# Performance work log

Measured on AMD Instinct MI355X. Metric: run time of the kernel, lower is better.

## Reference

```python
import jax, jax.numpy as jnp
import numpy as np

EPS = 1e-08
ATOM_CA = 1


def setup_inputs() -> dict:
    key = jax.random.key(0)
    k1, k2 = jax.random.split(key)
    B, N_RES, N_ATOMS = 256, 1024, 37
    pred_coords = jax.random.normal(k1, (B, N_RES, N_ATOMS, 3), dtype=jnp.float32)
    true_coords = jax.random.normal(k2, (B, N_RES, N_ATOMS, 3), dtype=jnp.float32)
    atom_mask = jnp.ones((B, N_RES, N_ATOMS), dtype=jnp.float32)
    return {"pred_coords": pred_coords, "true_coords": true_coords, "atom_mask": atom_mask}


def _kabsch_align(pred, true, mask):
    # pred/true: [B, N, 3], mask: [B, N]
    mask_sum = jnp.sum(mask, axis=1, keepdims=True) + EPS          # [B, 1]
    m = mask[..., None]                                             # [B, N, 1]
    pred_center = jnp.sum(pred * m, axis=1) / mask_sum              # [B, 3]
    true_center = jnp.sum(true * m, axis=1) / mask_sum              # [B, 3]
    pred_c = (pred - pred_center[:, None, :]) * m                   # [B, N, 3]
    true_c = (true - true_center[:, None, :]) * m                   # [B, N, 3]
    H = jnp.einsum('bni,bnj->bij', pred_c, true_c)                  # [B, 3, 3]
    U, s, Vh = jnp.linalg.svd(H)                                    # H = U diag(s) Vh
    V = jnp.swapaxes(Vh, -1, -2)
    Ut = jnp.swapaxes(U, -1, -2)
    det = jnp.linalg.det(jnp.matmul(V, Ut))                         # [B]
    sign = jnp.stack([jnp.ones_like(det), jnp.ones_like(det), det], axis=-1)  # [B, 3]
    S = jnp.eye(3, dtype=pred.dtype) * sign[:, None, :]             # diag(1,1,det)
    R = jnp.matmul(jnp.matmul(V, S), Ut)                            # [B, 3, 3]
    # aligned = (pred - pred_center) @ R^T + true_center
    aligned = jnp.einsum('bnj,bij->bni', pred - pred_center[:, None, :], R)
    return aligned + true_center[:, None, :]


def reference(pred_coords, true_coords, atom_mask):
    pred_ca = pred_coords[:, :, ATOM_CA, :]   # [B, N_res, 3]
    true_ca = true_coords[:, :, ATOM_CA, :]
    ca_mask = atom_mask[:, :, ATOM_CA]        # [B, N_res]
    pred_ca = _kabsch_align(pred_ca, true_ca, ca_mask)
    diff_sq = jnp.sum((pred_ca - true_ca) ** 2, axis=-1)            # [B, N_res]
    rmsd = jnp.sqrt(jnp.sum(diff_sq * ca_mask, axis=1) / (jnp.sum(ca_mask, axis=1) + EPS))
    return jnp.mean(rmsd)
```

## Files before the change

kernel.cpp:

```cpp
#include <hip/hip_runtime.h>
#include <math.h>

#define N_RES 1024
#define N_ATOMS 37
#define ATOM_CA 1
#define NBATCH 256
#define NSUM 34

__global__ __launch_bounds__(256) void rmsd_batch_kernel(
    const float* __restrict__ pred, const float* __restrict__ truec,
    const float* __restrict__ mask, float* __restrict__ ws)
{
    const int b = blockIdx.x;
    const int tid = threadIdx.x;

    float acc[NSUM];
#pragma unroll
    for (int i = 0; i < NSUM; ++i) acc[i] = 0.f;

    const size_t resStride = (size_t)N_ATOMS * 3;
    const float* pb = pred  + (size_t)b * N_RES * resStride + ATOM_CA * 3;
    const float* tb = truec + (size_t)b * N_RES * resStride + ATOM_CA * 3;
    const float* mb = mask  + (size_t)b * N_RES * N_ATOMS + ATOM_CA;

    for (int n = tid; n < N_RES; n += 256) {
        const float m  = mb[(size_t)n * N_ATOMS];
        const float* pp = pb + (size_t)n * resStride;
        const float* tt = tb + (size_t)n * resStride;
        const float p0 = pp[0], p1 = pp[1], p2 = pp[2];
        const float t0 = tt[0], t1 = tt[1], t2 = tt[2];
        const float m2 = m * m;
        acc[0] += m;
        acc[1] += m * p0;  acc[2] += m * p1;  acc[3] += m * p2;
        acc[4] += m * t0;  acc[5] += m * t1;  acc[6] += m * t2;
        acc[7] += m * (p0*p0 + p1*p1 + p2*p2);
        acc[8] += m * (t0*t0 + t1*t1 + t2*t2);
        acc[9]  += m * p0 * t0; acc[10] += m * p0 * t1; acc[11] += m * p0 * t2;
        acc[12] += m * p1 * t0; acc[13] += m * p1 * t1; acc[14] += m * p1 * t2;
        acc[15] += m * p2 * t0; acc[16] += m * p2 * t1; acc[17] += m * p2 * t2;
        acc[18] += m2;
        acc[19] += m2 * p0; acc[20] += m2 * p1; acc[21] += m2 * p2;
        acc[22] += m2 * t0; acc[23] += m2 * t1; acc[24] += m2 * t2;
        acc[25] += m2 * p0 * t0; acc[26] += m2 * p0 * t1; acc[27] += m2 * p0 * t2;
        acc[28] += m2 * p1 * t0; acc[29] += m2 * p1 * t1; acc[30] += m2 * p1 * t2;
        acc[31] += m2 * p2 * t0; acc[32] += m2 * p2 * t1; acc[33] += m2 * p2 * t2;
    }

#pragma unroll
    for (int i = 0; i < NSUM; ++i) {
        float v = acc[i];
#pragma unroll
        for (int off = 32; off > 0; off >>= 1) v += __shfl_down(v, off, 64);
        acc[i] = v;
    }

    __shared__ float partial[4][NSUM];
    __shared__ double sums[NSUM];
    const int wave = tid >> 6, lane = tid & 63;
    if (lane == 0) {
#pragma unroll
        for (int i = 0; i < NSUM; ++i) partial[wave][i] = acc[i];
    }
    __syncthreads();
    if (tid < NSUM) {
        sums[tid] = (double)partial[0][tid] + (double)partial[1][tid]
                  + (double)partial[2][tid] + (double)partial[3][tid];
    }
    __syncthreads();
    if (tid != 0) return;

    const double M   = sums[0];
    const double Mep = M + 1e-8;
    double Sp[3] = { sums[1], sums[2], sums[3] };
    double St[3] = { sums[4], sums[5], sums[6] };
    double pc[3] = { Sp[0] / Mep, Sp[1] / Mep, Sp[2] / Mep };
    double tc[3] = { St[0] / Mep, St[1] / Mep, St[2] / Mep };
    const double Qp = sums[7], Qt = sums[8];
    double Cpt[3][3];
    for (int i = 0; i < 3; ++i)
        for (int j = 0; j < 3; ++j) Cpt[i][j] = sums[9 + i * 3 + j];
    const double S2 = sums[18];
    double S2p[3] = { sums[19], sums[20], sums[21] };
    double S2t[3] = { sums[22], sums[23], sums[24] };
    double C2[3][3];
    for (int i = 0; i < 3; ++i)
        for (int j = 0; j < 3; ++j) C2[i][j] = sums[25 + i * 3 + j];

    double H[3][3];
    for (int i = 0; i < 3; ++i)
        for (int j = 0; j < 3; ++j)
            H[i][j] = C2[i][j] - pc[i] * S2t[j] - tc[j] * S2p[i] + pc[i] * tc[j] * S2;

    const double Sxx = H[0][0], Sxy = H[0][1], Sxz = H[0][2];
    const double Syx = H[1][0], Syy = H[1][1], Syz = H[1][2];
    const double Szx = H[2][0], Szy = H[2][1], Szz = H[2][2];
    double A[4][4] = {
        { Sxx + Syy + Szz, Syz - Szy,        Szx - Sxz,        Sxy - Syx },
        { Syz - Szy,       Sxx - Syy - Szz,  Sxy + Syx,        Szx + Sxz },
        { Szx - Sxz,       Sxy + Syx,       -Sxx + Syy - Szz,  Syz + Szy },
        { Sxy - Syx,       Szx + Sxz,        Syz + Szy,       -Sxx - Syy + Szz }
    };
    double Vm[4][4] = { {1,0,0,0},{0,1,0,0},{0,0,1,0},{0,0,0,1} };

    for (int sweep = 0; sweep < 16; ++sweep) {
        for (int p = 0; p < 3; ++p) {
            for (int q = p + 1; q < 4; ++q) {
                const double apq = A[p][q];
                if (fabs(apq) < 1e-30) continue;
                const double theta = (A[q][q] - A[p][p]) / (2.0 * apq);
                const double tt = (theta >= 0.0 ? 1.0 : -1.0)
                                / (fabs(theta) + sqrt(theta * theta + 1.0));
                const double c = 1.0 / sqrt(tt * tt + 1.0);
                const double s = tt * c;
                for (int k = 0; k < 4; ++k) {
                    const double akp = A[k][p], akq = A[k][q];
                    A[k][p] = c * akp - s * akq;
                    A[k][q] = s * akp + c * akq;
                }
                for (int k = 0; k < 4; ++k) {
                    const double apk = A[p][k], aqk = A[q][k];
                    A[p][k] = c * apk - s * aqk;
                    A[q][k] = s * apk + c * aqk;
                }
                for (int k = 0; k < 4; ++k) {
                    const double vkp = Vm[k][p], vkq = Vm[k][q];
                    Vm[k][p] = c * vkp - s * vkq;
                    Vm[k][q] = s * vkp + c * vkq;
                }
            }
        }
    }
    int best = 0;
    for (int i = 1; i < 4; ++i) if (A[i][i] > A[best][best]) best = i;
    double q0 = Vm[0][best], qx = Vm[1][best], qy = Vm[2][best], qz = Vm[3][best];
    const double nq = sqrt(q0*q0 + qx*qx + qy*qy + qz*qz);
    q0 /= nq; qx /= nq; qy /= nq; qz /= nq;

    double R[3][3] = {
        { 1 - 2*(qy*qy + qz*qz), 2*(qx*qy - qz*q0),     2*(qx*qz + qy*q0) },
        { 2*(qx*qy + qz*q0),     1 - 2*(qx*qx + qz*qz), 2*(qy*qz - qx*q0) },
        { 2*(qx*qz - qy*q0),     2*(qy*qz + qx*q0),     1 - 2*(qx*qx + qy*qy) }
    };

    double cross = 0.0;
    for (int i = 0; i < 3; ++i)
        for (int j = 0; j < 3; ++j) {
            const double Gij = Cpt[j][i] - tc[i] * Sp[j] - pc[j] * St[i]
                             + tc[i] * pc[j] * M;
            cross += R[i][j] * Gij;
        }

    const double Qpc = Qp - 2.0*(pc[0]*Sp[0] + pc[1]*Sp[1] + pc[2]*Sp[2])
                     + (pc[0]*pc[0] + pc[1]*pc[1] + pc[2]*pc[2]) * M;
    const double Qtc = Qt - 2.0*(tc[0]*St[0] + tc[1]*St[1] + tc[2]*St[2])
                     + (tc[0]*tc[0] + tc[1]*tc[1] + tc[2]*tc[2]) * M;
    double D = Qpc + Qtc - 2.0 * cross;
    if (D < 0.0) D = 0.0;
    ws[b] = (float)sqrt(D / Mep);
}

__global__ __launch_bounds__(256) void mean_kernel(const float* __restrict__ ws,
                                                   float* __restrict__ out)
{
    const int tid = threadIdx.x;
    float v = ws[tid];
#pragma unroll
    for (int off = 32; off > 0; off >>= 1) v += __shfl_down(v, off, 64);
    __shared__ float part[4];
    if ((tid & 63) == 0) part[tid >> 6] = v;
    __syncthreads();
    if (tid == 0)
        out[0] = (part[0] + part[1] + part[2] + part[3]) * (1.0f / (float)NBATCH);
}

extern "C" void kernel_launch(void* const* d_in, const int* in_sizes, int n_in,
                              void* d_out, int out_size, void* d_ws, size_t ws_size,
                              hipStream_t stream) {
    const float* pred  = (const float*)d_in[0];
    const float* truec = (const float*)d_in[1];
    const float* mask  = (const float*)d_in[2];
    float* out = (float*)d_out;
    float* ws  = (float*)d_ws;

    rmsd_batch_kernel<<<NBATCH, 256, 0, stream>>>(pred, truec, mask, ws);
    mean_kernel<<<1, 256, 0, stream>>>(ws, out);
}
```

Baseline: 252.3 us.

## Split moment accumulation across slices and solve eigenproblems in parallel fp32

The moment reduction is split into four residue slices per batch element (1024 blocks), and partial sums go to workspace. A single finish kernel then has each thread handle one batch element: it combines the partials, runs the quaternion Jacobi eigen-solve in fp32 with 8 unrolled sweeps instead of 16 fp64 sweeps, and reduces the mean. This removes the serial per-block thread-0 fp64 solve tail and raises memory parallelism, at the cost of reduced eigensolver precision.

```diff
diff --git a/kernel.cpp b/kernel.cpp
--- a/kernel.cpp
+++ b/kernel.cpp
@@ -5,46 +5,43 @@
 #define N_ATOMS 37
 #define ATOM_CA 1
 #define NBATCH 256
+#define SLICES 4
 #define NSUM 34
 
-__global__ __launch_bounds__(256) void rmsd_batch_kernel(
+__global__ __launch_bounds__(256) void rmsd_moments_kernel(
     const float* __restrict__ pred, const float* __restrict__ truec,
-    const float* __restrict__ mask, float* __restrict__ ws)
+    const float* __restrict__ mask, float* __restrict__ partials)
 {
-    const int b = blockIdx.x;
-    const int tid = threadIdx.x;
+    const int blk   = blockIdx.x;
+    const int b     = blk >> 2;
+    const int slice = blk & 3;
+    const int tid   = threadIdx.x;
+    const int n     = slice * 256 + tid;
+
+    const size_t resStride = (size_t)N_ATOMS * 3;
+    const float* pp = pred  + ((size_t)b * N_RES + n) * resStride + ATOM_CA * 3;
+    const float* tt = truec + ((size_t)b * N_RES + n) * resStride + ATOM_CA * 3;
+    const float  m  = mask[((size_t)b * N_RES + n) * N_ATOMS + ATOM_CA];
+
+    const float p0 = pp[0], p1 = pp[1], p2 = pp[2];
+    const float t0 = tt[0], t1 = tt[1], t2 = tt[2];
+    const float m2 = m * m;
 
     float acc[NSUM];
-#pragma unroll
-    for (int i = 0; i < NSUM; ++i) acc[i] = 0.f;
-
-    const size_t resStride = (size_t)N_ATOMS * 3;
-    const float* pb = pred  + (size_t)b * N_RES * resStride + ATOM_CA * 3;
-    const float* tb = truec + (size_t)b * N_RES * resStride + ATOM_CA * 3;
-    const float* mb = mask  + (size_t)b * N_RES * N_ATOMS + ATOM_CA;
-
-    for (int n = tid; n < N_RES; n += 256) {
-        const float m  = mb[(size_t)n * N_ATOMS];
-        const float* pp = pb + (size_t)n * resStride;
-        const float* tt = tb + (size_t)n * resStride;
-        const float p0 = pp[0], p1 = pp[1], p2 = pp[2];
-        const float t0 = tt[0], t1 = tt[1], t2 = tt[2];
-        const float m2 = m * m;
-        acc[0] += m;
-        acc[1] += m * p0;  acc[2] += m * p1;  acc[3] += m * p2;
-        acc[4] += m * t0;  acc[5] += m * t1;  acc[6] += m * t2;
-        acc[7] += m * (p0*p0 + p1*p1 + p2*p2);
-        acc[8] += m * (t0*t0 + t1*t1 + t2*t2);
-        acc[9]  += m * p0 * t0; acc[10] += m * p0 * t1; acc[11] += m * p0 * t2;
-        acc[12] += m * p1 * t0; acc[13] += m * p1 * t1; acc[14] += m * p1 * t2;
-        acc[15] += m * p2 * t0; acc[16] += m * p2 * t1; acc[17] += m * p2 * t2;
-        acc[18] += m2;
-        acc[19] += m2 * p0; acc[20] += m2 * p1; acc[21] += m2 * p2;
-        acc[22] += m2 * t0; acc[23] += m2 * t1; acc[24] += m2 * t2;
-        acc[25] += m2 * p0 * t0; acc[26] += m2 * p0 * t1; acc[27] += m2 * p0 * t2;
-        acc[28] += m2 * p1 * t0; acc[29] += m2 * p1 * t1; acc[30] += m2 * p1 * t2;
-        acc[31] += m2 * p2 * t0; acc[32] += m2 * p2 * t1; acc[33] += m2 * p2 * t2;
-    }
+    acc[0] = m;
+    acc[1] = m * p0;  acc[2] = m * p1;  acc[3] = m * p2;
+    acc[4] = m * t0;  acc[5] = m * t1;  acc[6] = m * t2;
+    acc[7] = m * (p0*p0 + p1*p1 + p2*p2);
+    acc[8] = m * (t0*t0 + t1*t1 + t2*t2);
+    acc[9]  = m * p0 * t0; acc[10] = m * p0 * t1; acc[11] = m * p0 * t2;
+    acc[12] = m * p1 * t0; acc[13] = m * p1 * t1; acc[14] = m * p1 * t2;
+    acc[15] = m * p2 * t0; acc[16] = m * p2 * t1; acc[17] = m * p2 * t2;
+    acc[18] = m2;
+    acc[19] = m2 * p0; acc[20] = m2 * p1; acc[21] = m2 * p2;
+    acc[22] = m2 * t0; acc[23] = m2 * t1; acc[24] = m2 * t2;
+    acc[25] = m2 * p0 * t0; acc[26] = m2 * p0 * t1; acc[27] = m2 * p0 * t2;
+    acc[28] = m2 * p1 * t0; acc[29] = m2 * p1 * t1; acc[30] = m2 * p1 * t2;
+    acc[31] = m2 * p2 * t0; acc[32] = m2 * p2 * t1; acc[33] = m2 * p2 * t2;
 
 #pragma unroll
     for (int i = 0; i < NSUM; ++i) {
@@ -55,7 +52,6 @@
     }
 
     __shared__ float partial[4][NSUM];
-    __shared__ double sums[NSUM];
     const int wave = tid >> 6, lane = tid & 63;
     if (lane == 0) {
 #pragma unroll
@@ -63,89 +59,110 @@
     }
     __syncthreads();
     if (tid < NSUM) {
-        sums[tid] = (double)partial[0][tid] + (double)partial[1][tid]
-                  + (double)partial[2][tid] + (double)partial[3][tid];
+        partials[(size_t)blk * NSUM + tid] =
+            partial[0][tid] + partial[1][tid] + partial[2][tid] + partial[3][tid];
     }
-    __syncthreads();
-    if (tid != 0) return;
+}
 
-    const double M   = sums[0];
+__global__ __launch_bounds__(256) void rmsd_finish_kernel(
+    const float* __restrict__ partials, float* __restrict__ out)
+{
+    const int b = threadIdx.x;
+
+    double s[NSUM];
+#pragma unroll
+    for (int i = 0; i < NSUM; ++i) s[i] = 0.0;
+#pragma unroll
+    for (int k = 0; k < SLICES; ++k) {
+        const float* row = partials + ((size_t)b * SLICES + k) * NSUM;
+#pragma unroll
+        for (int i = 0; i < NSUM; ++i) s[i] += (double)row[i];
+    }
+
+    const double M   = s[0];
     const double Mep = M + 1e-8;
-    double Sp[3] = { sums[1], sums[2], sums[3] };
-    double St[3] = { sums[4], sums[5], sums[6] };
+    double Sp[3] = { s[1], s[2], s[3] };
+    double St[3] = { s[4], s[5], s[6] };
     double pc[3] = { Sp[0] / Mep, Sp[1] / Mep, Sp[2] / Mep };
     double tc[3] = { St[0] / Mep, St[1] / Mep, St[2] / Mep };
-    const double Qp = sums[7], Qt = sums[8];
-    double Cpt[3][3];
-    for (int i = 0; i < 3; ++i)
-        for (int j = 0; j < 3; ++j) Cpt[i][j] = sums[9 + i * 3 + j];
-    const double S2 = sums[18];
-    double S2p[3] = { sums[19], sums[20], sums[21] };
-    double S2t[3] = { sums[22], sums[23], sums[24] };
-    double C2[3][3];
-    for (int i = 0; i < 3; ++i)
-        for (int j = 0; j < 3; ++j) C2[i][j] = sums[25 + i * 3 + j];
+    const double Qp = s[7], Qt = s[8];
+    const double S2 = s[18];
+    double S2p[3] = { s[19], s[20], s[21] };
+    double S2t[3] = { s[22], s[23], s[24] };
 
     double H[3][3];
+#pragma unroll
     for (int i = 0; i < 3; ++i)
+#pragma unroll
         for (int j = 0; j < 3; ++j)
-            H[i][j] = C2[i][j] - pc[i] * S2t[j] - tc[j] * S2p[i] + pc[i] * tc[j] * S2;
+            H[i][j] = s[25 + i * 3 + j] - pc[i] * S2t[j] - tc[j] * S2p[i]
+                    + pc[i] * tc[j] * S2;
 
-    const double Sxx = H[0][0], Sxy = H[0][1], Sxz = H[0][2];
-    const double Syx = H[1][0], Syy = H[1][1], Syz = H[1][2];
-    const double Szx = H[2][0], Szy = H[2][1], Szz = H[2][2];
-    double A[4][4] = {
+    const float Sxx = (float)H[0][0], Sxy = (float)H[0][1], Sxz = (float)H[0][2];
+    const float Syx = (float)H[1][0], Syy = (float)H[1][1], Syz = (float)H[1][2];
+    const float Szx = (float)H[2][0], Szy = (float)H[2][1], Szz = (float)H[2][2];
+    float A[4][4] = {
         { Sxx + Syy + Szz, Syz - Szy,        Szx - Sxz,        Sxy - Syx },
         { Syz - Szy,       Sxx - Syy - Szz,  Sxy + Syx,        Szx + Sxz },
         { Szx - Sxz,       Sxy + Syx,       -Sxx + Syy - Szz,  Syz + Szy },
         { Sxy - Syx,       Szx + Sxz,        Syz + Szy,       -Sxx - Syy + Szz }
     };
-    double Vm[4][4] = { {1,0,0,0},{0,1,0,0},{0,0,1,0},{0,0,0,1} };
+    float Vm[4][4] = { {1,0,0,0},{0,1,0,0},{0,0,1,0},{0,0,0,1} };
 
-    for (int sweep = 0; sweep < 16; ++sweep) {
+#pragma unroll
+    for (int sweep = 0; sweep < 8; ++sweep) {
+#pragma unroll
         for (int p = 0; p < 3; ++p) {
+#pragma unroll
             for (int q = p + 1; q < 4; ++q) {
-                const double apq = A[p][q];
-                if (fabs(apq) < 1e-30) continue;
-                const double theta = (A[q][q] - A[p][p]) / (2.0 * apq);
-                const double tt = (theta >= 0.0 ? 1.0 : -1.0)
-                                / (fabs(theta) + sqrt(theta * theta + 1.0));
-                const double c = 1.0 / sqrt(tt * tt + 1.0);
-                const double s = tt * c;
+                const float apq = A[p][q];
+                const float denom = fabsf(apq) > 1e-20f ? apq : 1e-20f;
+                const float theta = (A[q][q] - A[p][p]) / (2.0f * denom);
+                float tt = (theta >= 0.0f ? 1.0f : -1.0f)
+                         / (fabsf(theta) + sqrtf(theta * theta + 1.0f));
+                if (fabsf(apq) <= 1e-20f) tt = 0.0f;
+                const float c = 1.0f / sqrtf(tt * tt + 1.0f);
+                const float sn = tt * c;
+#pragma unroll
                 for (int k = 0; k < 4; ++k) {
-                    const double akp = A[k][p], akq = A[k][q];
-                    A[k][p] = c * akp - s * akq;
-                    A[k][q] = s * akp + c * akq;
+                    const float akp = A[k][p], akq = A[k][q];
+                    A[k][p] = c * akp - sn * akq;
+                    A[k][q] = sn * akp + c * akq;
                 }
+#pragma unroll
                 for (int k = 0; k < 4; ++k) {
-                    const double apk = A[p][k], aqk = A[q][k];
-                    A[p][k] = c * apk - s * aqk;
-                    A[q][k] = s * apk + c * aqk;
+                    const float apk = A[p][k], aqk = A[q][k];
+                    A[p][k] = c * apk - sn * aqk;
+                    A[q][k] = sn * apk + c * aqk;
                 }
+#pragma unroll
                 for (int k = 0; k < 4; ++k) {
-                    const double vkp = Vm[k][p], vkq = Vm[k][q];
-                    Vm[k][p] = c * vkp - s * vkq;
-                    Vm[k][q] = s * vkp + c * vkq;
+                    const float vkp = Vm[k][p], vkq = Vm[k][q];
+                    Vm[k][p] = c * vkp - sn * vkq;
+                    Vm[k][q] = sn * vkp + c * vkq;
                 }
             }
         }
     }
     int best = 0;
+#pragma unroll
     for (int i = 1; i < 4; ++i) if (A[i][i] > A[best][best]) best = i;
-    double q0 = Vm[0][best], qx = Vm[1][best], qy = Vm[2][best], qz = Vm[3][best];
-    const double nq = sqrt(q0*q0 + qx*qx + qy*qy + qz*qz);
+    float q0 = Vm[0][best], qx = Vm[1][best], qy = Vm[2][best], qz = Vm[3][best];
+    const float nq = sqrtf(q0*q0 + qx*qx + qy*qy + qz*qz);
     q0 /= nq; qx /= nq; qy /= nq; qz /= nq;
 
     double R[3][3] = {
-        { 1 - 2*(qy*qy + qz*qz), 2*(qx*qy - qz*q0),     2*(qx*qz + qy*q0) },
-        { 2*(qx*qy + qz*q0),     1 - 2*(qx*qx + qz*qz), 2*(qy*qz - qx*q0) },
-        { 2*(qx*qz - qy*q0),     2*(qy*qz + qx*q0),     1 - 2*(qx*qx + qy*qy) }
+        { 1.0 - 2.0*((double)qy*qy + (double)qz*qz), 2.0*((double)qx*qy - (double)qz*q0), 2.0*((double)qx*qz + (double)qy*q0) },
+        { 2.0*((double)qx*qy + (double)qz*q0), 1.0 - 2.0*((double)qx*qx + (double)qz*qz), 2.0*((double)qy*qz - (double)qx*q0) },
+        { 2.0*((double)qx*qz - (double)qy*q0), 2.0*((double)qy*qz + (double)qx*q0), 1.0 - 2.0*((double)qx*qx + (double)qy*qy) }
     };
 
     double cross = 0.0;
+#pragma unroll
     for (int i = 0; i < 3; ++i)
+#pragma unroll
         for (int j = 0; j < 3; ++j) {
-            const double Gij = Cpt[j][i] - tc[i] * Sp[j] - pc[j] * St[i]
+            const double Gij = s[9 + j * 3 + i] - tc[i] * Sp[j] - pc[j] * St[i]
                              + tc[i] * pc[j] * M;
             cross += R[i][j] * Gij;
         }
@@ -156,20 +173,14 @@
                      + (tc[0]*tc[0] + tc[1]*tc[1] + tc[2]*tc[2]) * M;
     double D = Qpc + Qtc - 2.0 * cross;
     if (D < 0.0) D = 0.0;
-    ws[b] = (float)sqrt(D / Mep);
-}
+    float rmsd = (float)sqrt(D / Mep);
 
-__global__ __launch_bounds__(256) void mean_kernel(const float* __restrict__ ws,
-                                                   float* __restrict__ out)
-{
-    const int tid = threadIdx.x;
-    float v = ws[tid];
 #pragma unroll
-    for (int off = 32; off > 0; off >>= 1) v += __shfl_down(v, off, 64);
+    for (int off = 32; off > 0; off >>= 1) rmsd += __shfl_down(rmsd, off, 64);
     __shared__ float part[4];
-    if ((tid & 63) == 0) part[tid >> 6] = v;
+    if ((threadIdx.x & 63) == 0) part[threadIdx.x >> 6] = rmsd;
     __syncthreads();
-    if (tid == 0)
+    if (threadIdx.x == 0)
         out[0] = (part[0] + part[1] + part[2] + part[3]) * (1.0f / (float)NBATCH);
 }
 
@@ -180,8 +191,8 @@
     const float* truec = (const float*)d_in[1];
     const float* mask  = (const float*)d_in[2];
     float* out = (float*)d_out;
-    float* ws  = (float*)d_ws;
+    float* partials = (float*)d_ws;
 
-    rmsd_batch_kernel<<<NBATCH, 256, 0, stream>>>(pred, truec, mask, ws);
-    mean_kernel<<<1, 256, 0, stream>>>(ws, out);
+    rmsd_moments_kernel<<<NBATCH * SLICES, 256, 0, stream>>>(pred, truec, mask, partials);
+    rmsd_finish_kernel<<<1, 256, 0, stream>>>(partials, out);
 }
```

Result: slower. 269.0 us (+6.6%).
